# Kernel optimization log

Measured on AMD Instinct MI355X. Metric: run time of the kernel, lower is better.

Reference implementation:

```python
import jax, jax.numpy as jnp
import numpy as np

D_MODEL = 1024
NHEAD = 16
D_K = D_MODEL // NHEAD


def setup_inputs() -> dict:
    key = jax.random.key(0)
    ks = jax.random.split(key, 12)
    B, L = 4, 2048
    s = 1.0 / np.sqrt(D_MODEL)
    inp = {
        "query": jax.random.normal(ks[0], (B, L, D_MODEL), jnp.float32),
        "key": jax.random.normal(ks[1], (B, L, D_MODEL), jnp.float32),
        "value": jax.random.normal(ks[2], (B, L, D_MODEL), jnp.float32),
        "Wq": jax.random.normal(ks[3], (D_MODEL, D_MODEL), jnp.float32) * s,
        "bq": jnp.zeros((D_MODEL,), jnp.float32),
        "Wk": jax.random.normal(ks[4], (D_MODEL, D_MODEL), jnp.float32) * s,
        "bk": jnp.zeros((D_MODEL,), jnp.float32),
        "Wv": jax.random.normal(ks[5], (D_MODEL, D_MODEL), jnp.float32) * s,
        "bv": jnp.zeros((D_MODEL,), jnp.float32),
        "Wo": jax.random.normal(ks[6], (D_MODEL, D_MODEL), jnp.float32) * s,
        "bo": jnp.zeros((D_MODEL,), jnp.float32),
    }
    return inp


def reference(query, key, value, Wq, bq, Wk, bk, Wv, bv, Wo, bo):
    B, Lq, _ = query.shape
    Lk = key.shape[1]
    # Linear projections, split into heads: [B, H, L, d_k]
    Q = (query @ Wq + bq).reshape(B, Lq, NHEAD, D_K).transpose(0, 2, 1, 3)
    K = (key @ Wk + bk).reshape(B, Lk, NHEAD, D_K).transpose(0, 2, 1, 3)
    V = (value @ Wv + bv).reshape(B, Lk, NHEAD, D_K).transpose(0, 2, 1, 3)
    scale = 1.0 / jnp.sqrt(jnp.asarray(D_K, Q.dtype))
    scores = jnp.einsum("bhqd,bhkd->bhqk", Q, K) * scale  # [B,H,Lq,Lk]
    attn = jax.nn.softmax(scores, axis=-1)
    context = jnp.einsum("bhqk,bhkd->bhqd", attn, V)
    context = context.transpose(0, 2, 1, 3).reshape(B, Lq, D_MODEL)
    return context @ Wo + bo
```

## Files before the change

### kernel.cpp

```cpp
#include <hip/hip_runtime.h>
#include <hip/hip_bf16.h>
#include <cstdint>
#include <cstddef>


typedef unsigned short u16;
typedef __bf16 bf8v __attribute__((ext_vector_type(8)));
typedef __bf16 bf4v __attribute__((ext_vector_type(4)));
typedef float f32x4 __attribute__((ext_vector_type(4)));

#define D_MODEL 1024
#define NHEAD   16
#define DK      64
#define BATCH   4
#define SEQ     2048
#define ROWS    (BATCH * SEQ)

__device__ __forceinline__ u16 f2b(float f) {
  union { float f; unsigned int i; } x; x.f = f;
  unsigned int r = x.i + 0x7fffu + ((x.i >> 16) & 1u);
  return (u16)(r >> 16);
}
__device__ __forceinline__ ushort4 pack4(float a, float b, float c, float d) {
  union { bf4v v; ushort4 u; } x;
  x.v[0] = (__bf16)a; x.v[1] = (__bf16)b; x.v[2] = (__bf16)c; x.v[3] = (__bf16)d;
  return x.u;
}
__device__ __forceinline__ bf8v cvt8(float4 a, float4 b) {
  bf8v r;
  r[0] = (__bf16)a.x; r[1] = (__bf16)a.y; r[2] = (__bf16)a.z; r[3] = (__bf16)a.w;
  r[4] = (__bf16)b.x; r[5] = (__bf16)b.y; r[6] = (__bf16)b.z; r[7] = (__bf16)b.w;
  return r;
}
__device__ __forceinline__ void async16(const void* g, void* l) {
  __builtin_amdgcn_global_load_lds((const __attribute__((address_space(1))) void*)g,
                                   (__attribute__((address_space(3))) void*)l, 16, 0, 0);
}
#define MFMA16(a, b, c) __builtin_amdgcn_mfma_f32_16x16x32_bf16(a, b, c, 0, 0, 0)

__global__ void wtrans_cvt_kernel(const float* __restrict__ w0, const float* __restrict__ w1,
                                  const float* __restrict__ w2, const float* __restrict__ w3,
                                  u16* __restrict__ dst4) {
  __shared__ float t[32][33];
  const float* src = (blockIdx.z == 0) ? w0 : (blockIdx.z == 1) ? w1
                   : (blockIdx.z == 2) ? w2 : w3;
  u16* dst = dst4 + (size_t)blockIdx.z * D_MODEL * D_MODEL;
  const int c0 = blockIdx.x * 32, r0 = blockIdx.y * 32;
  for (int i = threadIdx.y; i < 32; i += 8)
    t[i][threadIdx.x] = src[(size_t)(r0 + i) * D_MODEL + c0 + threadIdx.x];
  __syncthreads();
  for (int i = threadIdx.y; i < 32; i += 8)
    dst[(size_t)(c0 + i) * D_MODEL + r0 + threadIdx.x] = f2b(t[threadIdx.x][i]);
}

#define BM 128
#define BN 128
#define BK 64
#define NT (1024 / BK)

__global__ __launch_bounds__(256, 2) void gemm_qkv(
    const float* __restrict__ Aq, const float* __restrict__ Ak,
    const float* __restrict__ Av, const u16* __restrict__ wt,
    const float* __restrict__ bq, const float* __restrict__ bk,
    const float* __restrict__ bv, u16* __restrict__ Qw, u16* __restrict__ Kw,
    u16* __restrict__ Vt, float qscale) {
  __shared__ __align__(16) u16 As[2][BM * BK];
  __shared__ __align__(16) u16 Bs[2][BN * BK];
  const int z = blockIdx.y;
  const float* A = (z == 0) ? Aq : (z == 1) ? Ak : Av;
  const u16* Bt = wt + (size_t)z * D_MODEL * D_MODEL;
  const float* bias = (z == 0) ? bq : (z == 1) ? bk : bv;
  u16* out = (z == 0) ? Qw : (z == 1) ? Kw : Vt;
  const float oscale = (z == 0) ? qscale : 1.0f;

  const int lid = blockIdx.x;
  const int xcd = lid & 7, jj = lid >> 3;
  const int m0 = ((xcd << 3) + (jj >> 3)) * BM;
  const int n0 = (jj & 7) * BN;

  const int tid = threadIdx.x;
  const int lane = tid & 63, wave = tid >> 6;
  const int wm = wave >> 1, wn = wave & 1;
  const int quad = lane >> 4, l16 = lane & 15;
  const int K = 1024;

  f32x4 acc[4][4];
#pragma unroll
  for (int i = 0; i < 4; i++)
#pragma unroll
    for (int j = 0; j < 4; j++) acc[i][j] = (f32x4){0.f, 0.f, 0.f, 0.f};

  const int s8 = tid >> 3;
  const int lc = ((tid & 7) ^ ((tid >> 4) & 7)) * 8;
  const int fk = (l16 >> 1) & 7;
  const float* Agt = A + (size_t)(m0 + s8) * K + lc;
  const u16* Bgt = Bt + (size_t)(n0 + s8) * K + lc;

  float4 ar[8];
#pragma unroll
  for (int m = 0; m < 4; m++) {
    ar[2 * m]     = *(const float4*)(Agt + (size_t)m * 32 * K);
    ar[2 * m + 1] = *(const float4*)(Agt + (size_t)m * 32 * K + 4);
  }
#pragma unroll
  for (int m = 0; m < 4; m++)
    async16(Bgt + (size_t)m * 32 * K, &Bs[0][m * 2048 + tid * 8]);
#pragma unroll
  for (int m = 0; m < 4; m++)
    *(bf8v*)&As[0][m * 2048 + tid * 8] = cvt8(ar[2 * m], ar[2 * m + 1]);
#pragma unroll
  for (int m = 0; m < 4; m++) {
    ar[2 * m]     = *(const float4*)(Agt + (size_t)m * 32 * K + BK);
    ar[2 * m + 1] = *(const float4*)(Agt + (size_t)m * 32 * K + BK + 4);
  }
  __syncthreads();

  int p = 0;
  for (int t = 0; t < NT; t++) {
    const int kn = (t + 1) * BK;
    if (kn < K) {
#pragma unroll
      for (int m = 0; m < 4; m++)
        async16(Bgt + (size_t)m * 32 * K + kn, &Bs[p ^ 1][m * 2048 + tid * 8]);
#pragma unroll
      for (int m = 0; m < 4; m++)
        *(bf8v*)&As[p ^ 1][m * 2048 + tid * 8] = cvt8(ar[2 * m], ar[2 * m + 1]);
      if (kn + BK < K) {
#pragma unroll
        for (int m = 0; m < 4; m++) {
          ar[2 * m]     = *(const float4*)(Agt + (size_t)m * 32 * K + kn + BK);
          ar[2 * m + 1] = *(const float4*)(Agt + (size_t)m * 32 * K + kn + BK + 4);
        }
      }
    }

    bf8v af[4][2], bfr[4][2];
#pragma unroll
    for (int i = 0; i < 4; i++)
#pragma unroll
      for (int h = 0; h < 2; h++)
        af[i][h] = *(const bf8v*)&As[p][(wm * 64 + i * 16 + l16) * BK +
                                        (((h * 4 + quad) ^ fk) * 8)];
#pragma unroll
    for (int j = 0; j < 4; j++)
#pragma unroll
      for (int h = 0; h < 2; h++)
        bfr[j][h] = *(const bf8v*)&Bs[p][(wn * 64 + j * 16 + l16) * BK +
                                         (((h * 4 + quad) ^ fk) * 8)];
    __builtin_amdgcn_s_setprio(1);
    if (z < 2) {
#pragma unroll
      for (int i = 0; i < 4; i++)
#pragma unroll
        for (int j = 0; j < 4; j++) {
          acc[i][j] = MFMA16(bfr[j][0], af[i][0], acc[i][j]);
          acc[i][j] = MFMA16(bfr[j][1], af[i][1], acc[i][j]);
        }
    } else {
#pragma unroll
      for (int i = 0; i < 4; i++)
#pragma unroll
        for (int j = 0; j < 4; j++) {
          acc[i][j] = MFMA16(af[i][0], bfr[j][0], acc[i][j]);
          acc[i][j] = MFMA16(af[i][1], bfr[j][1], acc[i][j]);
        }
    }
    __builtin_amdgcn_s_setprio(0);
    __syncthreads();
    p ^= 1;
  }

  if (z < 2) {
#pragma unroll
    for (int i = 0; i < 4; i++) {
      const int m = m0 + wm * 64 + i * 16 + l16;
      const int b = m >> 11, l = m & 2047;
#pragma unroll
      for (int j = 0; j < 4; j++) {
        const int n = n0 + wn * 64 + j * 16 + quad * 4;
        const float4 bv4 = *(const float4*)&bias[n];
        const int h = n >> 6, d = n & 63;
        *(ushort4*)&out[(((size_t)(b * NHEAD + h) * SEQ + l) << 6) + d] =
            pack4((acc[i][j][0] + bv4.x) * oscale, (acc[i][j][1] + bv4.y) * oscale,
                  (acc[i][j][2] + bv4.z) * oscale, (acc[i][j][3] + bv4.w) * oscale);
      }
    }
  } else {
#pragma unroll
    for (int j = 0; j < 4; j++) {
      const int n = n0 + wn * 64 + j * 16 + l16;
      const float bvs = bias[n];
      const int h = n >> 6, d = n & 63;
#pragma unroll
      for (int i = 0; i < 4; i++) {
        const int row = m0 + wm * 64 + i * 16 + quad * 4;
        const int b = row >> 11, l = row & 2047;
        const int pl = (l & ~31) | ((l & 12) << 1) | ((l & 16) >> 2);
        *(ushort4*)&out[(((size_t)(b * NHEAD + h) * DK + d) << 11) + pl] =
            pack4(acc[i][j][0] + bvs, acc[i][j][1] + bvs,
                  acc[i][j][2] + bvs, acc[i][j][3] + bvs);
      }
    }
  }
}

__global__ __launch_bounds__(256, 2) void gemm_out(const u16* __restrict__ A,
                                                   const u16* __restrict__ Bt,
                                                   const float* __restrict__ bias,
                                                   float* __restrict__ out) {
  __shared__ __align__(16) u16 As[2][BM * BK];
  __shared__ __align__(16) u16 Bs[2][BN * BK];
  const int lid = blockIdx.x;
  const int xcd = lid & 7, jj = lid >> 3;
  const int m0 = ((xcd << 3) + (jj >> 3)) * BM;
  const int n0 = (jj & 7) * BN;
  const int tid = threadIdx.x;
  const int lane = tid & 63, wave = tid >> 6;
  const int wm = wave >> 1, wn = wave & 1;
  const int quad = lane >> 4, l16 = lane & 15;
  const int K = 1024;

  f32x4 acc[4][4];
#pragma unroll
  for (int i = 0; i < 4; i++)
#pragma unroll
    for (int j = 0; j < 4; j++) acc[i][j] = (f32x4){0.f, 0.f, 0.f, 0.f};

  const int s8 = tid >> 3;
  const int lc = ((tid & 7) ^ ((tid >> 4) & 7)) * 8;
  const int fk = (l16 >> 1) & 7;
  const u16* Agt = A + (size_t)(m0 + s8) * K + lc;
  const u16* Bgt = Bt + (size_t)(n0 + s8) * K + lc;

#pragma unroll
  for (int m = 0; m < 4; m++) {
    async16(Agt + (size_t)m * 32 * K, &As[0][m * 2048 + tid * 8]);
    async16(Bgt + (size_t)m * 32 * K, &Bs[0][m * 2048 + tid * 8]);
  }
  __syncthreads();

  int p = 0;
  for (int t = 0; t < NT; t++) {
    const int kn = (t + 1) * BK;
    if (kn < K) {
#pragma unroll
      for (int m = 0; m < 4; m++) {
        async16(Agt + (size_t)m * 32 * K + kn, &As[p ^ 1][m * 2048 + tid * 8]);
        async16(Bgt + (size_t)m * 32 * K + kn, &Bs[p ^ 1][m * 2048 + tid * 8]);
      }
    }

    bf8v af[4][2], bfr[4][2];
#pragma unroll
    for (int i = 0; i < 4; i++)
#pragma unroll
      for (int h = 0; h < 2; h++)
        af[i][h] = *(const bf8v*)&As[p][(wm * 64 + i * 16 + l16) * BK +
                                        (((h * 4 + quad) ^ fk) * 8)];
#pragma unroll
    for (int j = 0; j < 4; j++)
#pragma unroll
      for (int h = 0; h < 2; h++)
        bfr[j][h] = *(const bf8v*)&Bs[p][(wn * 64 + j * 16 + l16) * BK +
                                         (((h * 4 + quad) ^ fk) * 8)];
    __builtin_amdgcn_s_setprio(1);
#pragma unroll
    for (int i = 0; i < 4; i++)
#pragma unroll
      for (int j = 0; j < 4; j++) {
        acc[i][j] = MFMA16(bfr[j][0], af[i][0], acc[i][j]);
        acc[i][j] = MFMA16(bfr[j][1], af[i][1], acc[i][j]);
      }
    __builtin_amdgcn_s_setprio(0);
    __syncthreads();
    p ^= 1;
  }

#pragma unroll
  for (int i = 0; i < 4; i++) {
    const int m = m0 + wm * 64 + i * 16 + l16;
#pragma unroll
    for (int j = 0; j < 4; j++) {
      const int n = n0 + wn * 64 + j * 16 + quad * 4;
      const float4 bv4 = *(const float4*)&bias[n];
      float4 vv;
      vv.x = acc[i][j][0] + bv4.x; vv.y = acc[i][j][1] + bv4.y;
      vv.z = acc[i][j][2] + bv4.z; vv.w = acc[i][j][3] + bv4.w;
      *(float4*)&out[(size_t)m * D_MODEL + n] = vv;
    }
  }
}

__global__ __launch_bounds__(256, 4) void attn_kernel(const u16* __restrict__ Q,
                                                      const u16* __restrict__ K,
                                                      const u16* __restrict__ Vt,
                                                      u16* __restrict__ ctx) {
  const int bh = blockIdx.x;
  const int qb = blockIdx.y * 128;
  const int tid = threadIdx.x;
  const int lane = tid & 63, wave = tid >> 6;
  const int quad = lane >> 4, l16 = lane & 15;
  const u16* Qh = Q + (size_t)bh * SEQ * DK;
  const u16* Kh = K + (size_t)bh * SEQ * DK;
  const u16* Vh = Vt + (size_t)bh * DK * SEQ;

  __shared__ __align__(16) u16 Ks[2][2][64 * 32];
  __shared__ __align__(16) u16 Vs[2][64 * 64];

  const int srow = tid >> 2;
  const int sch  = ((tid & 3) ^ ((tid >> 3) & 3)) * 8;
  const int ldst = tid * 8;
  const int fsw  = (quad ^ ((l16 >> 1) & 3)) * 8;
  const int vd   = tid >> 3;
  const int vcol = ((tid & 7) ^ ((tid >> 3) & 7)) * 8;

  bf8v qf[2][2];
#pragma unroll
  for (int qg = 0; qg < 2; qg++)
#pragma unroll
    for (int h = 0; h < 2; h++)
      qf[qg][h] = *(const bf8v*)&Qh[(size_t)(qb + wave * 32 + qg * 16 + l16) * DK + h * 32 + quad * 8];

  bf8v ones;
#pragma unroll
  for (int j = 0; j < 8; j++) ones[j] = (__bf16)1.0f;

  f32x4 o[2][4];
  f32x4 la[2];
  float m_q[2];
#pragma unroll
  for (int qg = 0; qg < 2; qg++) {
    m_q[qg] = -1e30f; la[qg] = (f32x4){0.f, 0.f, 0.f, 0.f};
#pragma unroll
    for (int d = 0; d < 4; d++) o[qg][d] = (f32x4){0.f, 0.f, 0.f, 0.f};
  }

  async16(Kh + (size_t)srow * DK + sch,      &Ks[0][0][ldst]);
  async16(Kh + (size_t)srow * DK + 32 + sch, &Ks[0][1][ldst]);
  async16(Vh + (size_t)vd * SEQ + vcol,        &Vs[0][ldst]);
  async16(Vh + (size_t)(vd + 32) * SEQ + vcol, &Vs[0][2048 + ldst]);
  __syncthreads();

  int p = 0;
  for (int kt = 0; kt < SEQ; kt += 64) {
    const int nt = kt + 64;
    if (nt < SEQ) {
      async16(Kh + (size_t)(nt + srow) * DK + sch,      &Ks[p ^ 1][0][ldst]);
      async16(Kh + (size_t)(nt + srow) * DK + 32 + sch, &Ks[p ^ 1][1][ldst]);
      async16(Vh + (size_t)vd * SEQ + nt + vcol,        &Vs[p ^ 1][ldst]);
      async16(Vh + (size_t)(vd + 32) * SEQ + nt + vcol, &Vs[p ^ 1][2048 + ldst]);
    }

    bf8v kf[4][2];
#pragma unroll
    for (int nb = 0; nb < 4; nb++)
#pragma unroll
      for (int h = 0; h < 2; h++)
        kf[nb][h] = *(const bf8v*)&Ks[p][h][(nb * 16 + l16) * 32 + fsw];

    bf8v pf[2][2];
#pragma unroll
    for (int qg = 0; qg < 2; qg++) {
      f32x4 s[4];
      __builtin_amdgcn_s_setprio(1);
#pragma unroll
      for (int nb = 0; nb < 4; nb++) {
        f32x4 t = (f32x4){0.f, 0.f, 0.f, 0.f};
        t = MFMA16(kf[nb][0], qf[qg][0], t);
        t = MFMA16(kf[nb][1], qf[qg][1], t);
        s[nb] = t;
      }
      __builtin_amdgcn_s_setprio(0);
      float t0 = fmaxf(fmaxf(s[0][0], s[0][1]), fmaxf(s[0][2], s[0][3]));
      float t1 = fmaxf(fmaxf(s[1][0], s[1][1]), fmaxf(s[1][2], s[1][3]));
      float t2 = fmaxf(fmaxf(s[2][0], s[2][1]), fmaxf(s[2][2], s[2][3]));
      float t3 = fmaxf(fmaxf(s[3][0], s[3][1]), fmaxf(s[3][2], s[3][3]));
      float mx = fmaxf(fmaxf(t0, t1), fmaxf(t2, t3));
      mx = fmaxf(mx, __shfl_xor(mx, 16));
      mx = fmaxf(mx, __shfl_xor(mx, 32));
      const float mprev = m_q[qg];
      float Mn = mprev;
      const int resc = !__all(mx - mprev <= 8.0f);
      if (resc) {
        Mn = fmaxf(mprev, mx);
        const float al = __builtin_amdgcn_exp2f(mprev - Mn);
        m_q[qg] = Mn;
        la[qg] *= al;
#pragma unroll
        for (int d = 0; d < 4; d++) o[qg][d] *= al;
      }
#pragma unroll
      for (int nb = 0; nb < 4; nb++)
#pragma unroll
        for (int r = 0; r < 4; r++)
          s[nb][r] = __builtin_amdgcn_exp2f(s[nb][r] - Mn);
#pragma unroll
      for (int kc = 0; kc < 2; kc++) {
        bf8v pw;
#pragma unroll
        for (int j = 0; j < 4; j++) {
          pw[j]     = (__bf16)s[2 * kc][j];
          pw[j + 4] = (__bf16)s[2 * kc + 1][j];
        }
        pf[qg][kc] = pw;
      }
      la[qg] = MFMA16(ones, pf[qg][0], la[qg]);
      la[qg] = MFMA16(ones, pf[qg][1], la[qg]);
    }

    bf8v vf[4][2];
#pragma unroll
    for (int dc = 0; dc < 4; dc++) {
      const int rb = (dc * 16 + l16) * 64;
#pragma unroll
      for (int kc = 0; kc < 2; kc++)
        vf[dc][kc] = *(const bf8v*)&Vs[p][rb + (((kc * 4 + quad) ^ (l16 & 7)) * 8)];
    }
    __builtin_amdgcn_s_setprio(1);
#pragma unroll
    for (int qg = 0; qg < 2; qg++)
#pragma unroll
      for (int dc = 0; dc < 4; dc++) {
        o[qg][dc] = MFMA16(vf[dc][0], pf[qg][0], o[qg][dc]);
        o[qg][dc] = MFMA16(vf[dc][1], pf[qg][1], o[qg][dc]);
      }
    __builtin_amdgcn_s_setprio(0);

    __syncthreads();
    p ^= 1;
  }

  const int b = bh >> 4, hh = bh & 15;
#pragma unroll
  for (int qg = 0; qg < 2; qg++) {
    const float inv = __builtin_amdgcn_rcpf(la[qg][0]);
    const int q = qb + wave * 32 + qg * 16 + l16;
#pragma unroll
    for (int dc = 0; dc < 4; dc++) {
      const int col = hh * 64 + dc * 16 + quad * 4;
      *(ushort4*)&ctx[(size_t)(b * SEQ + q) * D_MODEL + col] =
          pack4(o[qg][dc][0] * inv, o[qg][dc][1] * inv,
                o[qg][dc][2] * inv, o[qg][dc][3] * inv);
    }
  }
}

extern "C" void kernel_launch(void* const* d_in, const int* in_sizes, int n_in,
                              void* d_out, int out_size, void* d_ws, size_t ws_size,
                              hipStream_t stream) {
  const float* q  = (const float*)d_in[0];
  const float* k  = (const float*)d_in[1];
  const float* v  = (const float*)d_in[2];
  const float* Wq = (const float*)d_in[3];
  const float* bq = (const float*)d_in[4];
  const float* Wk = (const float*)d_in[5];
  const float* bk = (const float*)d_in[6];
  const float* Wv = (const float*)d_in[7];
  const float* bv = (const float*)d_in[8];
  const float* Wo = (const float*)d_in[9];
  const float* bo = (const float*)d_in[10];

  u16* ws  = (u16*)d_ws;
  u16* wt  = ws;
  u16* Qw  = wt + (size_t)4 * D_MODEL * D_MODEL;
  u16* Kw  = Qw + (size_t)ROWS * D_MODEL;
  u16* Vt  = Kw + (size_t)ROWS * D_MODEL;
  u16* ctx = Vt + (size_t)ROWS * D_MODEL;

  const float QSCALE = 0.18033688011112042f;

  wtrans_cvt_kernel<<<dim3(32, 32, 4), dim3(32, 8), 0, stream>>>(Wq, Wk, Wv, Wo, wt);

  gemm_qkv<<<dim3(512, 3), 256, 0, stream>>>(q, k, v, wt, bq, bk, bv, Qw, Kw, Vt, QSCALE);

  attn_kernel<<<dim3(BATCH * NHEAD, SEQ / 128), 256, 0, stream>>>(Qw, Kw, Vt, ctx);

  gemm_out<<<512, 256, 0, stream>>>(ctx, wt + (size_t)3 * D_MODEL * D_MODEL, bo,
                                    (float*)d_out);
}
```

Baseline: 352.9 us.

## Use partial vmcnt waits in QKV GEMM, simplify output GEMM to single-buffer

In the QKV projection GEMM, the block-wide __syncthreads is replaced by a manual s_waitcnt vmcnt(8) plus s_barrier fenced with sched_barriers. The in-flight fp32 A prefetch for the next tile can then stay outstanding across the barrier instead of being drained each iteration. Separately, the output GEMM is rewritten to a simpler single-buffered BK=32 loop with a plain 2D grid. That version has no XCD remapping, no double buffering and scalar fp32 stores, so it loses load/compute overlap and store coalescing in the final projection.

```diff
diff --git a/kernel.cpp b/kernel.cpp
--- a/kernel.cpp
+++ b/kernel.cpp
@@ -55,8 +55,8 @@
 
 #define BM 128
 #define BN 128
-#define BK 64
-#define NT (1024 / BK)
+#define QBK 64
+#define QNT 16
 
 __global__ __launch_bounds__(256, 2) void gemm_qkv(
     const float* __restrict__ Aq, const float* __restrict__ Ak,
@@ -64,8 +64,8 @@
     const float* __restrict__ bq, const float* __restrict__ bk,
     const float* __restrict__ bv, u16* __restrict__ Qw, u16* __restrict__ Kw,
     u16* __restrict__ Vt, float qscale) {
-  __shared__ __align__(16) u16 As[2][BM * BK];
-  __shared__ __align__(16) u16 Bs[2][BN * BK];
+  __shared__ __align__(16) u16 As[2][BM * QBK];
+  __shared__ __align__(16) u16 Bs[2][BN * QBK];
   const int z = blockIdx.y;
   const float* A = (z == 0) ? Aq : (z == 1) ? Ak : Av;
   const u16* Bt = wt + (size_t)z * D_MODEL * D_MODEL;
@@ -110,26 +110,30 @@
     *(bf8v*)&As[0][m * 2048 + tid * 8] = cvt8(ar[2 * m], ar[2 * m + 1]);
 #pragma unroll
   for (int m = 0; m < 4; m++) {
-    ar[2 * m]     = *(const float4*)(Agt + (size_t)m * 32 * K + BK);
-    ar[2 * m + 1] = *(const float4*)(Agt + (size_t)m * 32 * K + BK + 4);
-  }
-  __syncthreads();
+    ar[2 * m]     = *(const float4*)(Agt + (size_t)m * 32 * K + QBK);
+    ar[2 * m + 1] = *(const float4*)(Agt + (size_t)m * 32 * K + QBK + 4);
+  }
+  __builtin_amdgcn_sched_barrier(0);
+  asm volatile("s_waitcnt vmcnt(8) lgkmcnt(0)" ::: "memory");
+  __builtin_amdgcn_s_barrier();
+  __builtin_amdgcn_sched_barrier(0);
 
   int p = 0;
-  for (int t = 0; t < NT; t++) {
-    const int kn = (t + 1) * BK;
-    if (kn < K) {
+  for (int t = 0; t < QNT; t++) {
+    if (t < QNT - 1) {
+      const int kn = (t + 1) * QBK;
 #pragma unroll
       for (int m = 0; m < 4; m++)
         async16(Bgt + (size_t)m * 32 * K + kn, &Bs[p ^ 1][m * 2048 + tid * 8]);
 #pragma unroll
       for (int m = 0; m < 4; m++)
         *(bf8v*)&As[p ^ 1][m * 2048 + tid * 8] = cvt8(ar[2 * m], ar[2 * m + 1]);
-      if (kn + BK < K) {
+      if (t < QNT - 2) {
+        const int ka = kn + QBK;
 #pragma unroll
         for (int m = 0; m < 4; m++) {
-          ar[2 * m]     = *(const float4*)(Agt + (size_t)m * 32 * K + kn + BK);
-          ar[2 * m + 1] = *(const float4*)(Agt + (size_t)m * 32 * K + kn + BK + 4);
+          ar[2 * m]     = *(const float4*)(Agt + (size_t)m * 32 * K + ka);
+          ar[2 * m + 1] = *(const float4*)(Agt + (size_t)m * 32 * K + ka + 4);
         }
       }
     }
@@ -139,13 +143,13 @@
     for (int i = 0; i < 4; i++)
 #pragma unroll
       for (int h = 0; h < 2; h++)
-        af[i][h] = *(const bf8v*)&As[p][(wm * 64 + i * 16 + l16) * BK +
+        af[i][h] = *(const bf8v*)&As[p][(wm * 64 + i * 16 + l16) * QBK +
                                         (((h * 4 + quad) ^ fk) * 8)];
 #pragma unroll
     for (int j = 0; j < 4; j++)
 #pragma unroll
       for (int h = 0; h < 2; h++)
-        bfr[j][h] = *(const bf8v*)&Bs[p][(wn * 64 + j * 16 + l16) * BK +
+        bfr[j][h] = *(const bf8v*)&Bs[p][(wn * 64 + j * 16 + l16) * QBK +
                                          (((h * 4 + quad) ^ fk) * 8)];
     __builtin_amdgcn_s_setprio(1);
     if (z < 2) {
@@ -166,7 +170,14 @@
         }
     }
     __builtin_amdgcn_s_setprio(0);
-    __syncthreads();
+
+    __builtin_amdgcn_sched_barrier(0);
+    if (t < QNT - 2)
+      asm volatile("s_waitcnt vmcnt(8) lgkmcnt(0)" ::: "memory");
+    else
+      asm volatile("s_waitcnt vmcnt(0) lgkmcnt(0)" ::: "memory");
+    __builtin_amdgcn_s_barrier();
+    __builtin_amdgcn_sched_barrier(0);
     p ^= 1;
   }
 
@@ -204,20 +215,19 @@
   }
 }
 
-__global__ __launch_bounds__(256, 2) void gemm_out(const u16* __restrict__ A,
-                                                   const u16* __restrict__ Bt,
-                                                   const float* __restrict__ bias,
-                                                   float* __restrict__ out) {
-  __shared__ __align__(16) u16 As[2][BM * BK];
-  __shared__ __align__(16) u16 Bs[2][BN * BK];
-  const int lid = blockIdx.x;
-  const int xcd = lid & 7, jj = lid >> 3;
-  const int m0 = ((xcd << 3) + (jj >> 3)) * BM;
-  const int n0 = (jj & 7) * BN;
+#define OBK 32
+
+__global__ __launch_bounds__(256) void gemm_out(const u16* __restrict__ A,
+                                                const u16* __restrict__ Bt,
+                                                const float* __restrict__ bias,
+                                                float* __restrict__ out) {
+  __shared__ __align__(16) u16 As[BM * OBK];
+  __shared__ __align__(16) u16 Bs[BN * OBK];
   const int tid = threadIdx.x;
   const int lane = tid & 63, wave = tid >> 6;
   const int wm = wave >> 1, wn = wave & 1;
   const int quad = lane >> 4, l16 = lane & 15;
+  const int m0 = blockIdx.x * BM, n0 = blockIdx.y * BN;
   const int K = 1024;
 
   f32x4 acc[4][4];
@@ -226,67 +236,46 @@
 #pragma unroll
     for (int j = 0; j < 4; j++) acc[i][j] = (f32x4){0.f, 0.f, 0.f, 0.f};
 
-  const int s8 = tid >> 3;
-  const int lc = ((tid & 7) ^ ((tid >> 4) & 7)) * 8;
-  const int fk = (l16 >> 1) & 7;
-  const u16* Agt = A + (size_t)(m0 + s8) * K + lc;
-  const u16* Bgt = Bt + (size_t)(n0 + s8) * K + lc;
-
-#pragma unroll
-  for (int m = 0; m < 4; m++) {
-    async16(Agt + (size_t)m * 32 * K, &As[0][m * 2048 + tid * 8]);
-    async16(Bgt + (size_t)m * 32 * K, &Bs[0][m * 2048 + tid * 8]);
-  }
-  __syncthreads();
-
-  int p = 0;
-  for (int t = 0; t < NT; t++) {
-    const int kn = (t + 1) * BK;
-    if (kn < K) {
-#pragma unroll
-      for (int m = 0; m < 4; m++) {
-        async16(Agt + (size_t)m * 32 * K + kn, &As[p ^ 1][m * 2048 + tid * 8]);
-        async16(Bgt + (size_t)m * 32 * K + kn, &Bs[p ^ 1][m * 2048 + tid * 8]);
-      }
-    }
-
-    bf8v af[4][2], bfr[4][2];
+  const int srow = tid >> 2;
+  const int sch = ((tid & 3) ^ ((tid >> 3) & 3)) * 8;
+  const int fsw = (quad ^ ((l16 >> 1) & 3)) * 8;
+  const u16* Ag = A + (size_t)(m0 + srow) * K + sch;
+  const u16* Bg = Bt + (size_t)(n0 + srow) * K + sch;
+
+  for (int k0 = 0; k0 < K; k0 += OBK) {
+    async16(Ag + k0, &As[tid * 8]);
+    async16(Ag + (size_t)64 * K + k0, &As[2048 + tid * 8]);
+    async16(Bg + k0, &Bs[tid * 8]);
+    async16(Bg + (size_t)64 * K + k0, &Bs[2048 + tid * 8]);
+    __syncthreads();
+
+    bf8v af[4], bfr[4];
 #pragma unroll
     for (int i = 0; i < 4; i++)
-#pragma unroll
-      for (int h = 0; h < 2; h++)
-        af[i][h] = *(const bf8v*)&As[p][(wm * 64 + i * 16 + l16) * BK +
-                                        (((h * 4 + quad) ^ fk) * 8)];
+      af[i] = *(const bf8v*)&As[(wm * 64 + i * 16 + l16) * OBK + fsw];
 #pragma unroll
     for (int j = 0; j < 4; j++)
-#pragma unroll
-      for (int h = 0; h < 2; h++)
-        bfr[j][h] = *(const bf8v*)&Bs[p][(wn * 64 + j * 16 + l16) * BK +
-                                         (((h * 4 + quad) ^ fk) * 8)];
-    __builtin_amdgcn_s_setprio(1);
+      bfr[j] = *(const bf8v*)&Bs[(wn * 64 + j * 16 + l16) * OBK + fsw];
 #pragma unroll
     for (int i = 0; i < 4; i++)
 #pragma unroll
-      for (int j = 0; j < 4; j++) {
-        acc[i][j] = MFMA16(bfr[j][0], af[i][0], acc[i][j]);
-        acc[i][j] = MFMA16(bfr[j][1], af[i][1], acc[i][j]);
-      }
-    __builtin_amdgcn_s_setprio(0);
+      for (int j = 0; j < 4; j++)
+        acc[i][j] = MFMA16(af[i], bfr[j], acc[i][j]);
     __syncthreads();
-    p ^= 1;
-  }
-
-#pragma unroll
-  for (int i = 0; i < 4; i++) {
-    const int m = m0 + wm * 64 + i * 16 + l16;
-#pragma unroll
-    for (int j = 0; j < 4; j++) {
-      const int n = n0 + wn * 64 + j * 16 + quad * 4;
-      const float4 bv4 = *(const float4*)&bias[n];
-      float4 vv;
-      vv.x = acc[i][j][0] + bv4.x; vv.y = acc[i][j][1] + bv4.y;
-      vv.z = acc[i][j][2] + bv4.z; vv.w = acc[i][j][3] + bv4.w;
-      *(float4*)&out[(size_t)m * D_MODEL + n] = vv;
+  }
+
+#pragma unroll
+  for (int j = 0; j < 4; j++) {
+    const int n = n0 + wn * 64 + j * 16 + l16;
+    const float bv = bias[n];
+#pragma unroll
+    for (int i = 0; i < 4; i++) {
+      const int gr0 = m0 + wm * 64 + i * 16 + quad * 4;
+#pragma unroll
+      for (int r = 0; r < 4; r++) {
+        const int row = gr0 + r;
+        out[(size_t)row * D_MODEL + n] = acc[i][j][r] + bv;
+      }
     }
   }
 }
@@ -475,6 +464,6 @@
 
   attn_kernel<<<dim3(BATCH * NHEAD, SEQ / 128), 256, 0, stream>>>(Qw, Kw, Vt, ctx);
 
-  gemm_out<<<512, 256, 0, stream>>>(ctx, wt + (size_t)3 * D_MODEL * D_MODEL, bo,
-                                    (float*)d_out);
-}
+  gemm_out<<<dim3(64, 8), 256, 0, stream>>>(ctx, wt + (size_t)3 * D_MODEL * D_MODEL,
+                                            bo, (float*)d_out);
+}
```

Measured after the change: 368.5 us. 1.04x slower.
